# Performance work log

Measured on AMD Instinct MI355X. Metric: run time of the kernel, lower is better.

Reference implementation:

```python
import jax, jax.numpy as jnp
import numpy as np

EPS = 1e-5
WBIT = 4
ABIT = 4

def _ste_round(x):
    return x + jax.lax.stop_gradient(jnp.round(x) - x)

def quantize_k(x, k):
    # uniform quantization to 2^k - 1 levels in [0,1], straight-through round
    n = float(2 ** k - 1)
    return _ste_round(x * n) / n

def weight_quant(w, k=WBIT):
    # DoReFa weight quantization (percentile=1.0 -> plain max)
    t = jnp.tanh(w)
    m = jnp.max(jnp.abs(t))
    wn = t / (2.0 * m) + 0.5            # in [0,1]
    return 2.0 * quantize_k(wn, k) - 1.0  # in [-1,1]

def act_quant(x, k=ABIT):
    return quantize_k(jnp.clip(x, 0.0, 1.0), k)

def bn(x, g, b, m, v):
    # inference batchnorm, per-channel (NCHW)
    scale = g / jnp.sqrt(v + EPS)
    return x * scale[None, :, None, None] + (b - m * scale)[None, :, None, None]

def conv(x, w, stride=1, pad=0, groups=1):
    return jax.lax.conv_general_dilated(
        x, w, window_strides=(stride, stride), padding=[(pad, pad), (pad, pad)],
        feature_group_count=groups, dimension_numbers=('NCHW', 'OIHW', 'NCHW'))

def setup_inputs() -> dict:
    key = jax.random.key(0)
    ks = jax.random.split(key, 17)
    N, Cin, H, W = 32, 64, 56, 56
    hidden = Cin * 6  # 384
    Cout = 64
    d = {
        'x':  jax.random.normal(ks[0], (N, Cin, H, W), jnp.float32),
        'w1': jax.random.normal(ks[1], (hidden, Cin, 1, 1), jnp.float32) * 0.1,
        'w2': jax.random.normal(ks[2], (hidden, 1, 3, 3), jnp.float32) * 0.1,
        'w3': jax.random.normal(ks[3], (Cout, hidden, 1, 1), jnp.float32) * 0.1,
        'g1': jax.random.uniform(ks[4], (hidden,), jnp.float32, 0.5, 1.5),
        'b1': jax.random.normal(ks[5], (hidden,), jnp.float32) * 0.1,
        'm1': jax.random.normal(ks[6], (hidden,), jnp.float32) * 0.1,
        'v1': jax.random.uniform(ks[7], (hidden,), jnp.float32, 0.5, 1.5),
        'g2': jax.random.uniform(ks[8], (hidden,), jnp.float32, 0.5, 1.5),
        'b2': jax.random.normal(ks[9], (hidden,), jnp.float32) * 0.1,
        'm2': jax.random.normal(ks[10], (hidden,), jnp.float32) * 0.1,
        'v2': jax.random.uniform(ks[11], (hidden,), jnp.float32, 0.5, 1.5),
        'g3': jax.random.uniform(ks[12], (Cout,), jnp.float32, 0.5, 1.5),
        'b3': jax.random.normal(ks[13], (Cout,), jnp.float32) * 0.1,
        'm3': jax.random.normal(ks[14], (Cout,), jnp.float32) * 0.1,
        'v3': jax.random.uniform(ks[15], (Cout,), jnp.float32, 0.5, 1.5),
    }
    return d

def reference(x, w1, w2, w3, g1, b1, m1, v1, g2, b2, m2, v2, g3, b3, m3, v3):
    hidden = w1.shape[0]
    shortcut = x
    h = act_quant(jax.nn.relu(bn(conv(x, weight_quant(w1)), g1, b1, m1, v1)))
    h = act_quant(jax.nn.relu(bn(conv(h, weight_quant(w2), stride=1, pad=1, groups=hidden), g2, b2, m2, v2)))
    h = act_quant(bn(conv(h, weight_quant(w3)), g3, b3, m3, v3))
    return h + shortcut  # stride==1 and in_planes==out_planes -> residual
```

## Files before the change

### kernel.cpp

```cpp
#include <hip/hip_runtime.h>
#include <hip/hip_bf16.h>

#define EPS 1e-5f
#define INV15 (1.0f/15.0f)

#define NB 32
#define CIN 64
#define HID 384
#define HH 56
#define HW 3136
#define NPIX 100352
#define BLKPB 1605632
#define NPIXU4 401408

#define OFF_BLOB1 0
#define OFF_W2PK 52224
#define OFF_A2   59136
#define OFF_B2   60672
#define OFF_BLOB3 62208
#define OFF_MAX  87296
#define OFF_H1 1048576
#define OFF_H2 20316160

typedef int v4i __attribute__((ext_vector_type(4)));
typedef float f32x4 __attribute__((ext_vector_type(4)));
typedef short bf16x8 __attribute__((ext_vector_type(8)));

__device__ __forceinline__ short splitbf(float f, float& rem) {
  __hip_bfloat16 h = __float2bfloat16(f);
  rem = f - __bfloat162float(h);
  return __builtin_bit_cast(short, h);
}

__device__ __forceinline__ int pk_mad(unsigned int w, int a, int c) {
  int d;
  asm("v_pk_mad_i16 %0, %1, %2, %3" : "=v"(d) : "v"(w), "v"(a), "v"(c));
  return d;
}

__device__ __forceinline__ int ch_of(int g, int j, int h) {
  return 32 * (g >> 2) + 4 * (g & 3) + 16 * (j & 1) + ((j >> 1) & 1) + 2 * h;
}

__global__ __launch_bounds__(256) void prep_max(
    const float* __restrict__ w1, const float* __restrict__ w2,
    const float* __restrict__ w3, unsigned int* __restrict__ maxout) {
  int b = blockIdx.x >> 4;
  int sub = blockIdx.x & 15;
  const float* src = (b == 0) ? w1 : (b == 1) ? w2 : w3;
  int n = (b == 1) ? HID * 9 : HID * CIN;
  float m = 0.f;
  for (int i = sub * 256 + threadIdx.x; i < n; i += 4096)
    m = fmaxf(m, fabsf(src[i]));
  #pragma unroll
  for (int off = 32; off > 0; off >>= 1)
    m = fmaxf(m, __shfl_down(m, off, 64));
  __shared__ float red[4];
  if ((threadIdx.x & 63) == 0) red[threadIdx.x >> 6] = m;
  __syncthreads();
  if (threadIdx.x == 0) {
    m = fmaxf(fmaxf(red[0], red[1]), fmaxf(red[2], red[3]));
    atomicMax(maxout + b, __float_as_uint(m));
  }
}

__global__ __launch_bounds__(256) void prep_quant(
    const float* __restrict__ w1, const float* __restrict__ w2,
    const float* __restrict__ w3,
    const float* __restrict__ g1, const float* __restrict__ b1,
    const float* __restrict__ m1, const float* __restrict__ v1,
    const float* __restrict__ g2, const float* __restrict__ b2,
    const float* __restrict__ m2, const float* __restrict__ v2,
    const float* __restrict__ g3, const float* __restrict__ b3,
    const float* __restrict__ m3, const float* __restrict__ v3,
    char* __restrict__ ws) {
  const float* maxv = (const float*)(ws + OFF_MAX);
  int idx = blockIdx.x * 256 + threadIdx.x;
  if (idx < 24576) {
    float mm = tanhf(maxv[0]);
    int e = idx & 7, lane = (idx >> 3) & 63, ks = (idx >> 9) & 1, mt = idx >> 10;
    int o = mt * 16 + (lane & 15);
    int k = ks * 32 + (lane >> 4) * 8 + e;
    float t = tanhf(w1[o * 64 + k]);
    int wi = 2 * (int)rintf((t / (2.f * mm) + 0.5f) * 15.f) - 15;
    float rr;
    ((short*)(ws + OFF_BLOB1))[idx] = splitbf((float)wi, rr);
  } else if (idx < 26304) {
    float mm = tanhf(maxv[1]);
    int jj = idx - 24576;
    int tap = jj / 192, rem = jj - tap * 192;
    int g = rem >> 2, j = rem & 3;
    int clo = ch_of(g, j, 0), chi = ch_of(g, j, 1);
    int wlo = 2 * (int)rintf((tanhf(w2[clo * 9 + tap]) / (2.f * mm) + 0.5f) * 15.f) - 15;
    int whi = 2 * (int)rintf((tanhf(w2[chi * 9 + tap]) / (2.f * mm) + 0.5f) * 15.f) - 15;
    ((unsigned int*)(ws + OFF_W2PK))[jj] =
        ((unsigned int)(unsigned short)(short)wlo) |
        (((unsigned int)(unsigned short)(short)whi) << 16);
  } else if (idx < 26688) {
    int ii = idx - 26304;
    int g = ii >> 3, j = (ii >> 1) & 3, h = ii & 1;
    int c = ch_of(g, j, h);
    float s = g2[c] / sqrtf(v2[c] + EPS);
    ((float*)(ws + OFF_A2))[ii] = s * (1.f / 15.f);
  } else if (idx < 27072) {
    int ii = idx - 26688;
    int g = ii >> 3, j = (ii >> 1) & 3, h = ii & 1;
    int c = ch_of(g, j, h);
    float s = g2[c] / sqrtf(v2[c] + EPS);
    ((float*)(ws + OFF_B2))[ii] = 15.f * (b2[c] - m2[c] * s) + 0.5f;
  } else if (idx < 27456) {
    int o = idx - 27072;
    ((float*)(ws + OFF_BLOB1 + 49152))[o] = g1[o] / sqrtf(v1[o] + EPS);
  } else if (idx < 27840) {
    int o = idx - 27456;
    float s = g1[o] / sqrtf(v1[o] + EPS);
    ((float*)(ws + OFF_BLOB1 + 50688))[o] = 15.f * (b1[o] - m1[o] * s);
  } else if (idx < 52416) {
    float mm = tanhf(maxv[2]);
    int jj = idx - 27840;
    int j = jj & 7, lane = (jj >> 3) & 63, nt = (jj >> 9) & 3, ks = jj >> 11;
    int n = nt * 16 + (lane & 15);
    int quad = lane >> 4;
    int k = ks * 32 + ((j & 1) ? (16 + quad * 4 + (j >> 1)) : (quad * 4 + (j >> 1)));
    float t = tanhf(w3[n * 384 + k]);
    int wi = 2 * (int)rintf((t / (2.f * mm) + 0.5f) * 15.f) - 15;
    (ws + OFF_BLOB3)[jj] = (char)wi;
  } else if (idx < 52480) {
    int n = idx - 52416;
    float s = g3[n] / sqrtf(v3[n] + EPS);
    *(float*)(ws + OFF_BLOB3 + 24576 + n * 4) = s * (1.f / 225.f);
  } else if (idx < 52544) {
    int n = idx - 52480;
    float s = g3[n] / sqrtf(v3[n] + EPS);
    *(float*)(ws + OFF_BLOB3 + 24832 + n * 4) = b3[n] - m3[n] * s;
  }
}

__global__ __launch_bounds__(256) void k1(
    const float* __restrict__ x, const char* __restrict__ blob1,
    char* __restrict__ h1b) {
  __shared__ uint4 sBuf[3264];
  int tid = threadIdx.x;
  {
    const uint4* src = (const uint4*)blob1;
    for (int i = tid; i < 3264; i += 256) sBuf[i] = src[i];
  }
  __syncthreads();
  const bf16x8* wf = (const bf16x8*)sBuf;
  const float* sSB = (const float*)(sBuf + 3072);

  int wv = tid >> 6, lane = tid & 63;
  int quad = lane >> 4, m = lane & 15;
  size_t pixabs = (size_t)blockIdx.x * 64 + wv * 16 + m;
  int img = blockIdx.x / 49;
  int prem = (blockIdx.x - img * 49) * 64 + wv * 16 + m;
  const float* xb = x + (size_t)img * (CIN * HW) + prem;

  bf16x8 xh[2], xl[2], xq[2];
  #pragma unroll
  for (int ks = 0; ks < 2; ks++) {
    #pragma unroll
    for (int e = 0; e < 8; e++) {
      float f = xb[(size_t)(ks * 32 + quad * 8 + e) * HW];
      float r1, r2, r3;
      xh[ks][e] = splitbf(f, r1);
      xl[ks][e] = splitbf(r1, r2);
      xq[ks][e] = splitbf(r2, r3);
    }
  }

  #pragma unroll
  for (int half = 0; half < 2; half++) {
    f32x4 acc[12];
    #pragma unroll
    for (int i = 0; i < 12; i++) { f32x4 z = {0.f, 0.f, 0.f, 0.f}; acc[i] = z; }
    #pragma unroll
    for (int i = 0; i < 12; i++) {
      int mt = half * 12 + i;
      bf16x8 w0 = wf[(mt * 2 + 0) * 64 + lane];
      bf16x8 w1 = wf[(mt * 2 + 1) * 64 + lane];
      acc[i] = __builtin_amdgcn_mfma_f32_16x16x32_bf16(w0, xh[0], acc[i], 0, 0, 0);
      acc[i] = __builtin_amdgcn_mfma_f32_16x16x32_bf16(w1, xh[1], acc[i], 0, 0, 0);
      acc[i] = __builtin_amdgcn_mfma_f32_16x16x32_bf16(w0, xl[0], acc[i], 0, 0, 0);
      acc[i] = __builtin_amdgcn_mfma_f32_16x16x32_bf16(w1, xl[1], acc[i], 0, 0, 0);
      acc[i] = __builtin_amdgcn_mfma_f32_16x16x32_bf16(w0, xq[0], acc[i], 0, 0, 0);
      acc[i] = __builtin_amdgcn_mfma_f32_16x16x32_bf16(w1, xq[1], acc[i], 0, 0, 0);
    }
    #pragma unroll
    for (int l = 0; l < 6; l++) {
      int b = half * 6 + l;
      f32x4 ae = acc[2 * l], ao = acc[2 * l + 1];
      unsigned int pk = 0;
      #pragma unroll
      for (int r = 0; r < 4; r++) {
        int oe = 32 * b + quad * 4 + r;
        int oo = oe + 16;
        float fe = fminf(fmaxf(ae[r] * sSB[oe] + sSB[384 + oe], 0.f), 15.f);
        float fo = fminf(fmaxf(ao[r] * sSB[oo] + sSB[384 + oo], 0.f), 15.f);
        pk |= ((unsigned int)(int)rintf(fe)) << (8 * r);
        pk |= ((unsigned int)(int)rintf(fo)) << (8 * r + 4);
      }
      *(unsigned int*)(h1b + (size_t)b * BLKPB + pixabs * 16 + quad * 4) = pk;
    }
  }
}

__global__ __launch_bounds__(256) void k2(
    const unsigned int* __restrict__ h1q, const char* __restrict__ wsrc,
    unsigned int* __restrict__ h2q) {
  __shared__ unsigned int sbuf[2496];
  int tid = threadIdx.x;
  for (int i = tid; i < 2496; i += 256) sbuf[i] = ((const unsigned int*)wsrc)[i];
  __syncthreads();
  const uint4* W4 = (const uint4*)sbuf;
  const float* Af = (const float*)(sbuf + 1728);
  const float* Bf = Af + 384;

  int g = blockIdx.y * 16 + (tid & 15);
  int qid = tid >> 4;
  int img = blockIdx.x / 49;
  int trem = blockIdx.x - img * 49;
  int px0 = trem * 64 + qid * 4;
  int h = px0 / 56;
  int w0 = px0 - h * 56;
  size_t base_u = (size_t)(g >> 2) * NPIXU4 + (g & 3);
  size_t imgrow = (size_t)img * HW;

  int acc[4][4];
  #pragma unroll
  for (int p = 0; p < 4; p++)
    #pragma unroll
    for (int j = 0; j < 4; j++) acc[p][j] = 0;

  #pragma unroll
  for (int dh = 0; dh < 3; dh++) {
    int hr = h + dh - 1;
    bool vrow = (unsigned)hr < 56u;
    const unsigned int* rp = h1q + base_u + (imgrow + (size_t)hr * 56) * 4;
    int P[6][4];
    #pragma unroll
    for (int c = 0; c < 6; c++) {
      int wc = w0 + c - 1;
      unsigned int u = 0;
      if (vrow && (unsigned)wc < 56u) u = rp[(size_t)wc * 4];
      P[c][0] = (int)(u & 0x000F000Fu);
      P[c][1] = (int)((u >> 4) & 0x000F000Fu);
      P[c][2] = (int)((u >> 8) & 0x000F000Fu);
      P[c][3] = (int)((u >> 12) & 0x000F000Fu);
    }
    #pragma unroll
    for (int cw = 0; cw < 3; cw++) {
      uint4 wvv = W4[(dh * 3 + cw) * 48 + g];
      #pragma unroll
      for (int p = 0; p < 4; p++) {
        acc[p][0] = pk_mad(wvv.x, P[p + cw][0], acc[p][0]);
        acc[p][1] = pk_mad(wvv.y, P[p + cw][1], acc[p][1]);
        acc[p][2] = pk_mad(wvv.z, P[p + cw][2], acc[p][2]);
        acc[p][3] = pk_mad(wvv.w, P[p + cw][3], acc[p][3]);
      }
    }
  }

  float Ar[8], Br[8];
  #pragma unroll
  for (int i = 0; i < 8; i++) { Ar[i] = Af[g * 8 + i]; Br[i] = Bf[g * 8 + i]; }

  #pragma unroll
  for (int p = 0; p < 4; p++) {
    unsigned int pk = 0;
    #pragma unroll
    for (int j = 0; j < 4; j++) {
      int a = acc[p][j];
      int lo = (a << 16) >> 16;
      int hi = a >> 16;
      float vl = fmaf((float)lo, Ar[2 * j], Br[2 * j]);
      float vh = fmaf((float)hi, Ar[2 * j + 1], Br[2 * j + 1]);
      unsigned int ql = (unsigned int)fmaxf(fminf(vl, 15.49f), 0.f);
      unsigned int qh = (unsigned int)fmaxf(fminf(vh, 15.49f), 0.f);
      pk |= ql << (4 * j);
      pk |= qh << (4 * j + 16);
    }
    h2q[base_u + (imgrow + (size_t)px0 + p) * 4] = pk;
  }
}

__global__ __launch_bounds__(256) void InvertedBottleneck_conv_Q_13709535609694_kernel(
    const unsigned int* __restrict__ h2q, const char* __restrict__ blob,
    const float* __restrict__ x, float* __restrict__ out) {
  __shared__ long lds8[3136];
  int tid = threadIdx.x;
  {
    const long* src = (const long*)blob;
    #pragma unroll
    for (int i = 0; i < 13; i++) {
      int j = tid + i * 256;
      if (j < 3136) lds8[j] = src[j];
    }
  }
  __syncthreads();

  int wv = tid >> 6;
  int lane = tid & 63;
  int m = lane & 15;
  int quad = lane >> 4;
  int pixW = blockIdx.x * 64 + wv * 16;

  const unsigned int* aptr = h2q + (size_t)(pixW + m) * 4 + quad;
  unsigned int ua[12];
  #pragma unroll
  for (int ks = 0; ks < 12; ks++) ua[ks] = aptr[(size_t)ks * NPIXU4];

  v4i acc[4];
  #pragma unroll
  for (int nt = 0; nt < 4; nt++) { v4i z = {0,0,0,0}; acc[nt] = z; }

  #pragma unroll
  for (int ks = 0; ks < 12; ks++) {
    unsigned int u = ua[ks];
    unsigned int t = u & 0x0F0F0F0Fu;
    unsigned int s = (u >> 4) & 0x0F0F0F0Fu;
    unsigned int d0 = (t & 0xFFu) | ((s & 0xFFu) << 8) | ((t & 0xFF00u) << 8) | ((s & 0xFF00u) << 16);
    unsigned int d1 = ((t >> 16) & 0xFFu) | (((s >> 16) & 0xFFu) << 8) | ((t >> 24) << 16) | ((s >> 24) << 24);
    long aF = (long)(((unsigned long)d1 << 32) | (unsigned long)d0);
    #pragma unroll
    for (int nt = 0; nt < 4; nt++) {
      long bF = lds8[(ks * 4 + nt) * 64 + lane];
      acc[nt] = __builtin_amdgcn_mfma_i32_16x16x32_i8(aF, bF, acc[nt], 0, 0, 0);
    }
  }

  const float* scl = (const float*)(lds8 + 3072);
  int img = blockIdx.x / 49;
  int prem = (blockIdx.x - img * 49) * 64 + wv * 16 + quad * 4;

  #pragma unroll
  for (int nt = 0; nt < 4; nt++) {
    int n = nt * 16 + m;
    float sc = scl[n];
    float bi = scl[64 + n];
    size_t off = ((size_t)img * CIN + n) * HW + prem;
    const float4 xv = *(const float4*)(x + off);
    float4 ov;
    float v, a;
    v = (float)acc[nt][0] * sc + bi; a = fminf(fmaxf(v, 0.f), 1.f); ov.x = rintf(a * 15.f) * INV15 + xv.x;
    v = (float)acc[nt][1] * sc + bi; a = fminf(fmaxf(v, 0.f), 1.f); ov.y = rintf(a * 15.f) * INV15 + xv.y;
    v = (float)acc[nt][2] * sc + bi; a = fminf(fmaxf(v, 0.f), 1.f); ov.z = rintf(a * 15.f) * INV15 + xv.z;
    v = (float)acc[nt][3] * sc + bi; a = fminf(fmaxf(v, 0.f), 1.f); ov.w = rintf(a * 15.f) * INV15 + xv.w;
    *(float4*)(out + off) = ov;
  }
}

extern "C" void kernel_launch(void* const* d_in, const int* in_sizes, int n_in,
                              void* d_out, int out_size, void* d_ws, size_t ws_size,
                              hipStream_t stream) {
  const float* x  = (const float*)d_in[0];
  const float* w1 = (const float*)d_in[1];
  const float* w2 = (const float*)d_in[2];
  const float* w3 = (const float*)d_in[3];
  const float* g1 = (const float*)d_in[4];
  const float* b1 = (const float*)d_in[5];
  const float* m1 = (const float*)d_in[6];
  const float* v1 = (const float*)d_in[7];
  const float* g2 = (const float*)d_in[8];
  const float* b2 = (const float*)d_in[9];
  const float* m2 = (const float*)d_in[10];
  const float* v2 = (const float*)d_in[11];
  const float* g3 = (const float*)d_in[12];
  const float* b3 = (const float*)d_in[13];
  const float* m3 = (const float*)d_in[14];
  const float* v3 = (const float*)d_in[15];

  char* ws = (char*)d_ws;
  unsigned int* maxu = (unsigned int*)(ws + OFF_MAX);
  char* h1b = ws + OFF_H1;
  char* h2b = ws + OFF_H2;
  float* outp = (float*)d_out;

  hipMemsetAsync(maxu, 0, 12, stream);
  prep_max<<<dim3(48), dim3(256), 0, stream>>>(w1, w2, w3, maxu);
  prep_quant<<<dim3(206), dim3(256), 0, stream>>>(
      w1, w2, w3, g1, b1, m1, v1, g2, b2, m2, v2, g3, b3, m3, v3, ws);
  k1<<<dim3(1568), dim3(256), 0, stream>>>(x, ws + OFF_BLOB1, h1b);
  k2<<<dim3(1568, 3), dim3(256), 0, stream>>>(
      (const unsigned int*)h1b, ws + OFF_W2PK, (unsigned int*)h2b);
  InvertedBottleneck_conv_Q_13709535609694_kernel<<<dim3(1568), dim3(256), 0, stream>>>(
      (const unsigned int*)h2b, ws + OFF_BLOB3, x, outp);
}
```

Before: 170.2 us.

## Fuse expand, depthwise and project stages into one kernel with LDS halo tiles

Replaces the three kernels (1x1 expand, 3x3 depthwise, 1x1 project) with one fused kernel. Each block handles two output rows of one image and recomputes a one-row halo above and below for the expand stage. The 4-bit hidden activations stay in shared memory instead of going through global workspace buffers. This removes the global write and read of h1 and h2 and two launches, at the cost of redundant halo compute, only 896 blocks, heavy register use (24 weight fragments, 48 B fragments) and extra barriers.

```diff
diff --git a/kernel.cpp b/kernel.cpp
--- a/kernel.cpp
+++ b/kernel.cpp
@@ -4,14 +4,9 @@
 #define EPS 1e-5f
 #define INV15 (1.0f/15.0f)
 
-#define NB 32
 #define CIN 64
 #define HID 384
-#define HH 56
 #define HW 3136
-#define NPIX 100352
-#define BLKPB 1605632
-#define NPIXU4 401408
 
 #define OFF_BLOB1 0
 #define OFF_W2PK 52224
@@ -19,8 +14,12 @@
 #define OFF_B2   60672
 #define OFF_BLOB3 62208
 #define OFF_MAX  87296
-#define OFF_H1 1048576
-#define OFF_H2 20316160
+
+#define SH_H1 0
+#define SH_K2 11200
+#define SH_S1 13696
+#define SH_SC3 14464
+#define SH_TOT 14592
 
 typedef int v4i __attribute__((ext_vector_type(4)));
 typedef float f32x4 __attribute__((ext_vector_type(4)));
@@ -136,217 +135,220 @@
   }
 }
 
-__global__ __launch_bounds__(256) void k1(
-    const float* __restrict__ x, const char* __restrict__ blob1,
-    char* __restrict__ h1b) {
-  __shared__ uint4 sBuf[3264];
+__global__ __launch_bounds__(256, 2) void InvertedBottleneck_conv_Q_13709535609694_kernel(
+    const float* __restrict__ x, const char* __restrict__ ws,
+    float* __restrict__ out) {
+  __shared__ unsigned int sh[SH_TOT];
   int tid = threadIdx.x;
   {
-    const uint4* src = (const uint4*)blob1;
-    for (int i = tid; i < 3264; i += 256) sBuf[i] = src[i];
-  }
-  __syncthreads();
-  const bf16x8* wf = (const bf16x8*)sBuf;
-  const float* sSB = (const float*)(sBuf + 3072);
+    const unsigned int* s2 = (const unsigned int*)(ws + OFF_W2PK);
+    for (int i = tid; i < 2496; i += 256) sh[SH_K2 + i] = s2[i];
+    const unsigned int* s1 = (const unsigned int*)(ws + OFF_BLOB1 + 49152);
+    for (int i = tid; i < 768; i += 256) sh[SH_S1 + i] = s1[i];
+    const unsigned int* s3 = (const unsigned int*)(ws + OFF_BLOB3 + 24576);
+    if (tid < 128) sh[SH_SC3 + tid] = s3[tid];
+  }
 
   int wv = tid >> 6, lane = tid & 63;
   int quad = lane >> 4, m = lane & 15;
-  size_t pixabs = (size_t)blockIdx.x * 64 + wv * 16 + m;
-  int img = blockIdx.x / 49;
-  int prem = (blockIdx.x - img * 49) * 64 + wv * 16 + m;
-  const float* xb = x + (size_t)img * (CIN * HW) + prem;
-
-  bf16x8 xh[2], xl[2], xq[2];
+  int img = blockIdx.x / 28;
+  int tileid = blockIdx.x - img * 28;
+  int r0 = tileid * 2;
+
+  const float* xb = x + (size_t)img * (CIN * HW);
+  const bf16x8* w1g = (const bf16x8*)(ws + OFF_BLOB1);
+
+  __syncthreads();
+
+  const float* sc15 = (const float*)&sh[SH_S1];
   #pragma unroll
-  for (int ks = 0; ks < 2; ks++) {
-    #pragma unroll
-    for (int e = 0; e < 8; e++) {
-      float f = xb[(size_t)(ks * 32 + quad * 8 + e) * HW];
-      float r1, r2, r3;
-      xh[ks][e] = splitbf(f, r1);
-      xl[ks][e] = splitbf(r1, r2);
-      xq[ks][e] = splitbf(r2, r3);
-    }
-  }
-
-  #pragma unroll
-  for (int half = 0; half < 2; half++) {
-    f32x4 acc[12];
-    #pragma unroll
-    for (int i = 0; i < 12; i++) { f32x4 z = {0.f, 0.f, 0.f, 0.f}; acc[i] = z; }
+  for (int mh = 0; mh < 2; mh++) {
+    bf16x8 wfr[24];
     #pragma unroll
     for (int i = 0; i < 12; i++) {
-      int mt = half * 12 + i;
-      bf16x8 w0 = wf[(mt * 2 + 0) * 64 + lane];
-      bf16x8 w1 = wf[(mt * 2 + 1) * 64 + lane];
-      acc[i] = __builtin_amdgcn_mfma_f32_16x16x32_bf16(w0, xh[0], acc[i], 0, 0, 0);
-      acc[i] = __builtin_amdgcn_mfma_f32_16x16x32_bf16(w1, xh[1], acc[i], 0, 0, 0);
-      acc[i] = __builtin_amdgcn_mfma_f32_16x16x32_bf16(w0, xl[0], acc[i], 0, 0, 0);
-      acc[i] = __builtin_amdgcn_mfma_f32_16x16x32_bf16(w1, xl[1], acc[i], 0, 0, 0);
-      acc[i] = __builtin_amdgcn_mfma_f32_16x16x32_bf16(w0, xq[0], acc[i], 0, 0, 0);
-      acc[i] = __builtin_amdgcn_mfma_f32_16x16x32_bf16(w1, xq[1], acc[i], 0, 0, 0);
+      wfr[2 * i]     = w1g[((mh * 12 + i) * 2 + 0) * 64 + lane];
+      wfr[2 * i + 1] = w1g[((mh * 12 + i) * 2 + 1) * 64 + lane];
     }
+    for (int it = 0; it < 4; it++) {
+      int tile = wv + 4 * it;
+      int px_local = tile * 16 + m;
+      int gpx = r0 * 56 - 56 + px_local;
+      gpx = (gpx < 0) ? 0 : ((gpx > HW - 1) ? HW - 1 : gpx);
+      bf16x8 xh[2], xl[2], xq[2];
+      #pragma unroll
+      for (int ks = 0; ks < 2; ks++) {
+        #pragma unroll
+        for (int e = 0; e < 8; e++) {
+          float f = xb[(size_t)(ks * 32 + quad * 8 + e) * HW + gpx];
+          float r1, r2, r3;
+          xh[ks][e] = splitbf(f, r1);
+          xl[ks][e] = splitbf(r1, r2);
+          xq[ks][e] = splitbf(r2, r3);
+        }
+      }
+      f32x4 acc[12];
+      #pragma unroll
+      for (int i = 0; i < 12; i++) { f32x4 z = {0.f, 0.f, 0.f, 0.f}; acc[i] = z; }
+      #pragma unroll
+      for (int i = 0; i < 12; i++) acc[i] = __builtin_amdgcn_mfma_f32_16x16x32_bf16(wfr[2*i],   xh[0], acc[i], 0, 0, 0);
+      #pragma unroll
+      for (int i = 0; i < 12; i++) acc[i] = __builtin_amdgcn_mfma_f32_16x16x32_bf16(wfr[2*i+1], xh[1], acc[i], 0, 0, 0);
+      #pragma unroll
+      for (int i = 0; i < 12; i++) acc[i] = __builtin_amdgcn_mfma_f32_16x16x32_bf16(wfr[2*i],   xl[0], acc[i], 0, 0, 0);
+      #pragma unroll
+      for (int i = 0; i < 12; i++) acc[i] = __builtin_amdgcn_mfma_f32_16x16x32_bf16(wfr[2*i+1], xl[1], acc[i], 0, 0, 0);
+      #pragma unroll
+      for (int i = 0; i < 12; i++) acc[i] = __builtin_amdgcn_mfma_f32_16x16x32_bf16(wfr[2*i],   xq[0], acc[i], 0, 0, 0);
+      #pragma unroll
+      for (int i = 0; i < 12; i++) acc[i] = __builtin_amdgcn_mfma_f32_16x16x32_bf16(wfr[2*i+1], xq[1], acc[i], 0, 0, 0);
+      if (px_local < 224) {
+        #pragma unroll
+        for (int l = 0; l < 6; l++) {
+          int b = mh * 6 + l;
+          f32x4 ae = acc[2 * l], ao = acc[2 * l + 1];
+          unsigned int pk = 0;
+          #pragma unroll
+          for (int r = 0; r < 4; r++) {
+            int oe = 32 * b + quad * 4 + r;
+            int oo = oe + 16;
+            float fe = fminf(fmaxf(ae[r] * sc15[oe] + sc15[384 + oe], 0.f), 15.f);
+            float fo = fminf(fmaxf(ao[r] * sc15[oo] + sc15[384 + oo], 0.f), 15.f);
+            pk |= ((unsigned int)(int)rintf(fe)) << (8 * r);
+            pk |= ((unsigned int)(int)rintf(fo)) << (8 * r + 4);
+          }
+          sh[SH_H1 + px_local * 50 + b * 4 + quad] = pk;
+        }
+      }
+    }
+  }
+  __syncthreads();
+
+  {
+    const uint4* W4 = (const uint4*)&sh[SH_K2];
+    const float* Af = (const float*)&sh[SH_K2 + 1728];
+    const float* Bf = Af + 384;
     #pragma unroll
-    for (int l = 0; l < 6; l++) {
-      int b = half * 6 + l;
-      f32x4 ae = acc[2 * l], ao = acc[2 * l + 1];
-      unsigned int pk = 0;
-      #pragma unroll
-      for (int r = 0; r < 4; r++) {
-        int oe = 32 * b + quad * 4 + r;
-        int oo = oe + 16;
-        float fe = fminf(fmaxf(ae[r] * sSB[oe] + sSB[384 + oe], 0.f), 15.f);
-        float fo = fminf(fmaxf(ao[r] * sSB[oo] + sSB[384 + oo], 0.f), 15.f);
-        pk |= ((unsigned int)(int)rintf(fe)) << (8 * r);
-        pk |= ((unsigned int)(int)rintf(fo)) << (8 * r + 4);
-      }
-      *(unsigned int*)(h1b + (size_t)b * BLKPB + pixabs * 16 + quad * 4) = pk;
+    for (int orow = 0; orow < 2; orow++) {
+      unsigned int opk[3][4];
+      #pragma unroll
+      for (int it2 = 0; it2 < 3; it2++) {
+        int id = it2 * 256 + tid;
+        int gg = id % 48, q = id / 48;
+        bool act = id < 672;
+        int col = q * 4;
+        int acc2[4][4];
+        #pragma unroll
+        for (int p = 0; p < 4; p++)
+          #pragma unroll
+          for (int j = 0; j < 4; j++) acc2[p][j] = 0;
+        #pragma unroll
+        for (int dh = 0; dh < 3; dh++) {
+          int grow = r0 - 1 + orow + dh;
+          bool vrow = (unsigned)grow < 56u;
+          int P[6][4];
+          #pragma unroll
+          for (int c = 0; c < 6; c++) {
+            int wc = col + c - 1;
+            unsigned int u = 0;
+            if (act && vrow && (unsigned)wc < 56u)
+              u = sh[SH_H1 + ((orow + dh) * 56 + wc) * 50 + gg];
+            P[c][0] = (int)(u & 0x000F000Fu);
+            P[c][1] = (int)((u >> 4) & 0x000F000Fu);
+            P[c][2] = (int)((u >> 8) & 0x000F000Fu);
+            P[c][3] = (int)((u >> 12) & 0x000F000Fu);
+          }
+          #pragma unroll
+          for (int cw = 0; cw < 3; cw++) {
+            uint4 wvv = W4[(dh * 3 + cw) * 48 + gg];
+            #pragma unroll
+            for (int p = 0; p < 4; p++) {
+              acc2[p][0] = pk_mad(wvv.x, P[p + cw][0], acc2[p][0]);
+              acc2[p][1] = pk_mad(wvv.y, P[p + cw][1], acc2[p][1]);
+              acc2[p][2] = pk_mad(wvv.z, P[p + cw][2], acc2[p][2]);
+              acc2[p][3] = pk_mad(wvv.w, P[p + cw][3], acc2[p][3]);
+            }
+          }
+        }
+        float Ar[8], Br[8];
+        #pragma unroll
+        for (int i = 0; i < 8; i++) { Ar[i] = Af[gg * 8 + i]; Br[i] = Bf[gg * 8 + i]; }
+        #pragma unroll
+        for (int p = 0; p < 4; p++) {
+          unsigned int pk = 0;
+          #pragma unroll
+          for (int j = 0; j < 4; j++) {
+            int a = acc2[p][j];
+            int lo = (a << 16) >> 16;
+            int hi = a >> 16;
+            float vl = fmaf((float)lo, Ar[2 * j], Br[2 * j]);
+            float vh = fmaf((float)hi, Ar[2 * j + 1], Br[2 * j + 1]);
+            unsigned int ql = (unsigned int)fmaxf(fminf(vl, 15.49f), 0.f);
+            unsigned int qh = (unsigned int)fmaxf(fminf(vh, 15.49f), 0.f);
+            pk |= ql << (4 * j);
+            pk |= qh << (4 * j + 16);
+          }
+          opk[it2][p] = pk;
+        }
+      }
+      __syncthreads();
+      #pragma unroll
+      for (int it2 = 0; it2 < 3; it2++) {
+        int id = it2 * 256 + tid;
+        int gg = id % 48, q = id / 48;
+        if (id < 672) {
+          #pragma unroll
+          for (int p = 0; p < 4; p++)
+            sh[SH_H1 + (orow * 56 + q * 4 + p) * 50 + gg] = opk[it2][p];
+        }
+      }
+      __syncthreads();
     }
   }
-}
-
-__global__ __launch_bounds__(256) void k2(
-    const unsigned int* __restrict__ h1q, const char* __restrict__ wsrc,
-    unsigned int* __restrict__ h2q) {
-  __shared__ unsigned int sbuf[2496];
-  int tid = threadIdx.x;
-  for (int i = tid; i < 2496; i += 256) sbuf[i] = ((const unsigned int*)wsrc)[i];
-  __syncthreads();
-  const uint4* W4 = (const uint4*)sbuf;
-  const float* Af = (const float*)(sbuf + 1728);
-  const float* Bf = Af + 384;
-
-  int g = blockIdx.y * 16 + (tid & 15);
-  int qid = tid >> 4;
-  int img = blockIdx.x / 49;
-  int trem = blockIdx.x - img * 49;
-  int px0 = trem * 64 + qid * 4;
-  int h = px0 / 56;
-  int w0 = px0 - h * 56;
-  size_t base_u = (size_t)(g >> 2) * NPIXU4 + (g & 3);
-  size_t imgrow = (size_t)img * HW;
-
-  int acc[4][4];
-  #pragma unroll
-  for (int p = 0; p < 4; p++)
+
+  {
+    const unsigned long long* w3g = (const unsigned long long*)(ws + OFF_BLOB3);
+    long bfr[48];
     #pragma unroll
-    for (int j = 0; j < 4; j++) acc[p][j] = 0;
-
-  #pragma unroll
-  for (int dh = 0; dh < 3; dh++) {
-    int hr = h + dh - 1;
-    bool vrow = (unsigned)hr < 56u;
-    const unsigned int* rp = h1q + base_u + (imgrow + (size_t)hr * 56) * 4;
-    int P[6][4];
-    #pragma unroll
-    for (int c = 0; c < 6; c++) {
-      int wc = w0 + c - 1;
-      unsigned int u = 0;
-      if (vrow && (unsigned)wc < 56u) u = rp[(size_t)wc * 4];
-      P[c][0] = (int)(u & 0x000F000Fu);
-      P[c][1] = (int)((u >> 4) & 0x000F000Fu);
-      P[c][2] = (int)((u >> 8) & 0x000F000Fu);
-      P[c][3] = (int)((u >> 12) & 0x000F000Fu);
+    for (int ci = 0; ci < 48; ci++) bfr[ci] = (long)w3g[ci * 64 + lane];
+    const float* scl = (const float*)&sh[SH_SC3];
+
+    for (int t = wv; t < 7; t += 4) {
+      int px = t * 16 + m;
+      unsigned int ua[12];
+      #pragma unroll
+      for (int ks = 0; ks < 12; ks++) ua[ks] = sh[SH_H1 + px * 50 + ks * 4 + quad];
+      v4i acc3[4];
+      #pragma unroll
+      for (int nt = 0; nt < 4; nt++) { v4i z = {0, 0, 0, 0}; acc3[nt] = z; }
+      #pragma unroll
+      for (int ks = 0; ks < 12; ks++) {
+        unsigned int u = ua[ks];
+        unsigned int tt = u & 0x0F0F0F0Fu;
+        unsigned int ss = (u >> 4) & 0x0F0F0F0Fu;
+        unsigned int d0 = (tt & 0xFFu) | ((ss & 0xFFu) << 8) | ((tt & 0xFF00u) << 8) | ((ss & 0xFF00u) << 16);
+        unsigned int d1 = ((tt >> 16) & 0xFFu) | (((ss >> 16) & 0xFFu) << 8) | ((tt >> 24) << 16) | ((ss >> 24) << 24);
+        long aF = (long)(((unsigned long)d1 << 32) | (unsigned long)d0);
+        #pragma unroll
+        for (int nt = 0; nt < 4; nt++)
+          acc3[nt] = __builtin_amdgcn_mfma_i32_16x16x32_i8(aF, bfr[ks * 4 + nt], acc3[nt], 0, 0, 0);
+      }
+      int prem = r0 * 56 + t * 16 + quad * 4;
+      #pragma unroll
+      for (int nt = 0; nt < 4; nt++) {
+        int n = nt * 16 + m;
+        float sc = scl[n];
+        float bi = scl[64 + n];
+        size_t off = ((size_t)img * CIN + n) * HW + prem;
+        const float4 xv = *(const float4*)(x + off);
+        float4 ov;
+        float v, a;
+        v = (float)acc3[nt][0] * sc + bi; a = fminf(fmaxf(v, 0.f), 1.f); ov.x = rintf(a * 15.f) * INV15 + xv.x;
+        v = (float)acc3[nt][1] * sc + bi; a = fminf(fmaxf(v, 0.f), 1.f); ov.y = rintf(a * 15.f) * INV15 + xv.y;
+        v = (float)acc3[nt][2] * sc + bi; a = fminf(fmaxf(v, 0.f), 1.f); ov.z = rintf(a * 15.f) * INV15 + xv.z;
+        v = (float)acc3[nt][3] * sc + bi; a = fminf(fmaxf(v, 0.f), 1.f); ov.w = rintf(a * 15.f) * INV15 + xv.w;
+        *(float4*)(out + off) = ov;
+      }
     }
-    #pragma unroll
-    for (int cw = 0; cw < 3; cw++) {
-      uint4 wvv = W4[(dh * 3 + cw) * 48 + g];
-      #pragma unroll
-      for (int p = 0; p < 4; p++) {
-        acc[p][0] = pk_mad(wvv.x, P[p + cw][0], acc[p][0]);
-        acc[p][1] = pk_mad(wvv.y, P[p + cw][1], acc[p][1]);
-        acc[p][2] = pk_mad(wvv.z, P[p + cw][2], acc[p][2]);
-        acc[p][3] = pk_mad(wvv.w, P[p + cw][3], acc[p][3]);
-      }
-    }
-  }
-
-  float Ar[8], Br[8];
-  #pragma unroll
-  for (int i = 0; i < 8; i++) { Ar[i] = Af[g * 8 + i]; Br[i] = Bf[g * 8 + i]; }
-
-  #pragma unroll
-  for (int p = 0; p < 4; p++) {
-    unsigned int pk = 0;
-    #pragma unroll
-    for (int j = 0; j < 4; j++) {
-      int a = acc[p][j];
-      int lo = (a << 16) >> 16;
-      int hi = a >> 16;
-      float vl = fmaf((float)lo, Ar[2 * j], Br[2 * j]);
-      float vh = fmaf((float)hi, Ar[2 * j + 1], Br[2 * j + 1]);
-      unsigned int ql = (unsigned int)fmaxf(fminf(vl, 15.49f), 0.f);
-      unsigned int qh = (unsigned int)fmaxf(fminf(vh, 15.49f), 0.f);
-      pk |= ql << (4 * j);
-      pk |= qh << (4 * j + 16);
-    }
-    h2q[base_u + (imgrow + (size_t)px0 + p) * 4] = pk;
-  }
-}
-
-__global__ __launch_bounds__(256) void InvertedBottleneck_conv_Q_13709535609694_kernel(
-    const unsigned int* __restrict__ h2q, const char* __restrict__ blob,
-    const float* __restrict__ x, float* __restrict__ out) {
-  __shared__ long lds8[3136];
-  int tid = threadIdx.x;
-  {
-    const long* src = (const long*)blob;
-    #pragma unroll
-    for (int i = 0; i < 13; i++) {
-      int j = tid + i * 256;
-      if (j < 3136) lds8[j] = src[j];
-    }
-  }
-  __syncthreads();
-
-  int wv = tid >> 6;
-  int lane = tid & 63;
-  int m = lane & 15;
-  int quad = lane >> 4;
-  int pixW = blockIdx.x * 64 + wv * 16;
-
-  const unsigned int* aptr = h2q + (size_t)(pixW + m) * 4 + quad;
-  unsigned int ua[12];
-  #pragma unroll
-  for (int ks = 0; ks < 12; ks++) ua[ks] = aptr[(size_t)ks * NPIXU4];
-
-  v4i acc[4];
-  #pragma unroll
-  for (int nt = 0; nt < 4; nt++) { v4i z = {0,0,0,0}; acc[nt] = z; }
-
-  #pragma unroll
-  for (int ks = 0; ks < 12; ks++) {
-    unsigned int u = ua[ks];
-    unsigned int t = u & 0x0F0F0F0Fu;
-    unsigned int s = (u >> 4) & 0x0F0F0F0Fu;
-    unsigned int d0 = (t & 0xFFu) | ((s & 0xFFu) << 8) | ((t & 0xFF00u) << 8) | ((s & 0xFF00u) << 16);
-    unsigned int d1 = ((t >> 16) & 0xFFu) | (((s >> 16) & 0xFFu) << 8) | ((t >> 24) << 16) | ((s >> 24) << 24);
-    long aF = (long)(((unsigned long)d1 << 32) | (unsigned long)d0);
-    #pragma unroll
-    for (int nt = 0; nt < 4; nt++) {
-      long bF = lds8[(ks * 4 + nt) * 64 + lane];
-      acc[nt] = __builtin_amdgcn_mfma_i32_16x16x32_i8(aF, bF, acc[nt], 0, 0, 0);
-    }
-  }
-
-  const float* scl = (const float*)(lds8 + 3072);
-  int img = blockIdx.x / 49;
-  int prem = (blockIdx.x - img * 49) * 64 + wv * 16 + quad * 4;
-
-  #pragma unroll
-  for (int nt = 0; nt < 4; nt++) {
-    int n = nt * 16 + m;
-    float sc = scl[n];
-    float bi = scl[64 + n];
-    size_t off = ((size_t)img * CIN + n) * HW + prem;
-    const float4 xv = *(const float4*)(x + off);
-    float4 ov;
-    float v, a;
-    v = (float)acc[nt][0] * sc + bi; a = fminf(fmaxf(v, 0.f), 1.f); ov.x = rintf(a * 15.f) * INV15 + xv.x;
-    v = (float)acc[nt][1] * sc + bi; a = fminf(fmaxf(v, 0.f), 1.f); ov.y = rintf(a * 15.f) * INV15 + xv.y;
-    v = (float)acc[nt][2] * sc + bi; a = fminf(fmaxf(v, 0.f), 1.f); ov.z = rintf(a * 15.f) * INV15 + xv.z;
-    v = (float)acc[nt][3] * sc + bi; a = fminf(fmaxf(v, 0.f), 1.f); ov.w = rintf(a * 15.f) * INV15 + xv.w;
-    *(float4*)(out + off) = ov;
   }
 }
 
@@ -372,17 +374,12 @@
 
   char* ws = (char*)d_ws;
   unsigned int* maxu = (unsigned int*)(ws + OFF_MAX);
-  char* h1b = ws + OFF_H1;
-  char* h2b = ws + OFF_H2;
   float* outp = (float*)d_out;
 
   hipMemsetAsync(maxu, 0, 12, stream);
   prep_max<<<dim3(48), dim3(256), 0, stream>>>(w1, w2, w3, maxu);
   prep_quant<<<dim3(206), dim3(256), 0, stream>>>(
       w1, w2, w3, g1, b1, m1, v1, g2, b2, m2, v2, g3, b3, m3, v3, ws);
-  k1<<<dim3(1568), dim3(256), 0, stream>>>(x, ws + OFF_BLOB1, h1b);
-  k2<<<dim3(1568, 3), dim3(256), 0, stream>>>(
-      (const unsigned int*)h1b, ws + OFF_W2PK, (unsigned int*)h2b);
-  InvertedBottleneck_conv_Q_13709535609694_kernel<<<dim3(1568), dim3(256), 0, stream>>>(
-      (const unsigned int*)h2b, ws + OFF_BLOB3, x, outp);
-}
+  InvertedBottleneck_conv_Q_13709535609694_kernel<<<dim3(896), dim3(256), 0, stream>>>(
+      x, ws, outp);
+}
```

Result: slower. 185.0 us (+8.7%).

## Fuse depthwise conv into final pointwise conv via shared-memory h2 tile

Applied to the files above, without the earlier changes.

Merges the depthwise 3x3 kernel into the final 1x1 conv kernel. Each block now computes the 64-pixel, 384-channel h2 tile, stores it in LDS and feeds the int8 MFMA directly, so the h2 intermediate never makes a global-memory round trip. k1 is also changed to process two 16-pixel groups per wave with half the grid, reusing the staged weights. The cost is more LDS per block (about 48KB), which lowers occupancy, plus serialization between the depthwise and MFMA phases within a block.

```diff
diff --git a/kernel.cpp b/kernel.cpp
--- a/kernel.cpp
+++ b/kernel.cpp
@@ -4,10 +4,8 @@
 #define EPS 1e-5f
 #define INV15 (1.0f/15.0f)
 
-#define NB 32
 #define CIN 64
 #define HID 384
-#define HH 56
 #define HW 3136
 #define NPIX 100352
 #define BLKPB 1605632
@@ -20,7 +18,12 @@
 #define OFF_BLOB3 62208
 #define OFF_MAX  87296
 #define OFF_H1 1048576
-#define OFF_H2 20316160
+
+#define SH_W2 0
+#define SH_W3 2496
+#define SH_SC3 8640
+#define SH_H2 8768
+#define SH_TOT 11968
 
 typedef int v4i __attribute__((ext_vector_type(4)));
 typedef float f32x4 __attribute__((ext_vector_type(4)));
@@ -151,202 +154,195 @@
 
   int wv = tid >> 6, lane = tid & 63;
   int quad = lane >> 4, m = lane & 15;
-  size_t pixabs = (size_t)blockIdx.x * 64 + wv * 16 + m;
-  int img = blockIdx.x / 49;
-  int prem = (blockIdx.x - img * 49) * 64 + wv * 16 + m;
-  const float* xb = x + (size_t)img * (CIN * HW) + prem;
-
-  bf16x8 xh[2], xl[2], xq[2];
-  #pragma unroll
-  for (int ks = 0; ks < 2; ks++) {
-    #pragma unroll
-    for (int e = 0; e < 8; e++) {
-      float f = xb[(size_t)(ks * 32 + quad * 8 + e) * HW];
-      float r1, r2, r3;
-      xh[ks][e] = splitbf(f, r1);
-      xl[ks][e] = splitbf(r1, r2);
-      xq[ks][e] = splitbf(r2, r3);
-    }
-  }
-
-  #pragma unroll
-  for (int half = 0; half < 2; half++) {
-    f32x4 acc[12];
-    #pragma unroll
-    for (int i = 0; i < 12; i++) { f32x4 z = {0.f, 0.f, 0.f, 0.f}; acc[i] = z; }
-    #pragma unroll
-    for (int i = 0; i < 12; i++) {
-      int mt = half * 12 + i;
-      bf16x8 w0 = wf[(mt * 2 + 0) * 64 + lane];
-      bf16x8 w1 = wf[(mt * 2 + 1) * 64 + lane];
-      acc[i] = __builtin_amdgcn_mfma_f32_16x16x32_bf16(w0, xh[0], acc[i], 0, 0, 0);
-      acc[i] = __builtin_amdgcn_mfma_f32_16x16x32_bf16(w1, xh[1], acc[i], 0, 0, 0);
-      acc[i] = __builtin_amdgcn_mfma_f32_16x16x32_bf16(w0, xl[0], acc[i], 0, 0, 0);
-      acc[i] = __builtin_amdgcn_mfma_f32_16x16x32_bf16(w1, xl[1], acc[i], 0, 0, 0);
-      acc[i] = __builtin_amdgcn_mfma_f32_16x16x32_bf16(w0, xq[0], acc[i], 0, 0, 0);
-      acc[i] = __builtin_amdgcn_mfma_f32_16x16x32_bf16(w1, xq[1], acc[i], 0, 0, 0);
-    }
-    #pragma unroll
-    for (int l = 0; l < 6; l++) {
-      int b = half * 6 + l;
-      f32x4 ae = acc[2 * l], ao = acc[2 * l + 1];
-      unsigned int pk = 0;
-      #pragma unroll
-      for (int r = 0; r < 4; r++) {
-        int oe = 32 * b + quad * 4 + r;
-        int oo = oe + 16;
-        float fe = fminf(fmaxf(ae[r] * sSB[oe] + sSB[384 + oe], 0.f), 15.f);
-        float fo = fminf(fmaxf(ao[r] * sSB[oo] + sSB[384 + oo], 0.f), 15.f);
-        pk |= ((unsigned int)(int)rintf(fe)) << (8 * r);
-        pk |= ((unsigned int)(int)rintf(fo)) << (8 * r + 4);
-      }
-      *(unsigned int*)(h1b + (size_t)b * BLKPB + pixabs * 16 + quad * 4) = pk;
-    }
-  }
-}
-
-__global__ __launch_bounds__(256) void k2(
-    const unsigned int* __restrict__ h1q, const char* __restrict__ wsrc,
-    unsigned int* __restrict__ h2q) {
-  __shared__ unsigned int sbuf[2496];
+
+  for (int t = 0; t < 2; t++) {
+    int grp = blockIdx.x * 8 + t * 4 + wv;
+    size_t pixabs = (size_t)grp * 16 + m;
+    int img = grp / 196;
+    int prem = (grp - img * 196) * 16 + m;
+    const float* xb = x + (size_t)img * (CIN * HW) + prem;
+
+    bf16x8 xh[2], xl[2], xq[2];
+    #pragma unroll
+    for (int ks = 0; ks < 2; ks++) {
+      #pragma unroll
+      for (int e = 0; e < 8; e++) {
+        float f = xb[(size_t)(ks * 32 + quad * 8 + e) * HW];
+        float r1, r2, r3;
+        xh[ks][e] = splitbf(f, r1);
+        xl[ks][e] = splitbf(r1, r2);
+        xq[ks][e] = splitbf(r2, r3);
+      }
+    }
+
+    #pragma unroll
+    for (int half = 0; half < 2; half++) {
+      f32x4 acc[12];
+      #pragma unroll
+      for (int i = 0; i < 12; i++) { f32x4 z = {0.f, 0.f, 0.f, 0.f}; acc[i] = z; }
+      #pragma unroll
+      for (int i = 0; i < 12; i++) {
+        int mt = half * 12 + i;
+        bf16x8 w0 = wf[(mt * 2 + 0) * 64 + lane];
+        bf16x8 w1 = wf[(mt * 2 + 1) * 64 + lane];
+        acc[i] = __builtin_amdgcn_mfma_f32_16x16x32_bf16(w0, xh[0], acc[i], 0, 0, 0);
+        acc[i] = __builtin_amdgcn_mfma_f32_16x16x32_bf16(w1, xh[1], acc[i], 0, 0, 0);
+        acc[i] = __builtin_amdgcn_mfma_f32_16x16x32_bf16(w0, xl[0], acc[i], 0, 0, 0);
+        acc[i] = __builtin_amdgcn_mfma_f32_16x16x32_bf16(w1, xl[1], acc[i], 0, 0, 0);
+        acc[i] = __builtin_amdgcn_mfma_f32_16x16x32_bf16(w0, xq[0], acc[i], 0, 0, 0);
+        acc[i] = __builtin_amdgcn_mfma_f32_16x16x32_bf16(w1, xq[1], acc[i], 0, 0, 0);
+      }
+      #pragma unroll
+      for (int l = 0; l < 6; l++) {
+        int b = half * 6 + l;
+        f32x4 ae = acc[2 * l], ao = acc[2 * l + 1];
+        unsigned int pk = 0;
+        #pragma unroll
+        for (int r = 0; r < 4; r++) {
+          int oe = 32 * b + quad * 4 + r;
+          int oo = oe + 16;
+          float fe = fminf(fmaxf(ae[r] * sSB[oe] + sSB[384 + oe], 0.f), 15.f);
+          float fo = fminf(fmaxf(ao[r] * sSB[oo] + sSB[384 + oo], 0.f), 15.f);
+          pk |= ((unsigned int)(int)rintf(fe)) << (8 * r);
+          pk |= ((unsigned int)(int)rintf(fo)) << (8 * r + 4);
+        }
+        *(unsigned int*)(h1b + (size_t)b * BLKPB + pixabs * 16 + quad * 4) = pk;
+      }
+    }
+  }
+}
+
+__global__ __launch_bounds__(256) void InvertedBottleneck_conv_Q_13709535609694_kernel(
+    const unsigned int* __restrict__ h1q, const char* __restrict__ ws,
+    const float* __restrict__ x, float* __restrict__ out) {
+  __shared__ unsigned int sh[SH_TOT];
   int tid = threadIdx.x;
-  for (int i = tid; i < 2496; i += 256) sbuf[i] = ((const unsigned int*)wsrc)[i];
+  {
+    const unsigned int* s2 = (const unsigned int*)(ws + OFF_W2PK);
+    for (int i = tid; i < 2496; i += 256) sh[SH_W2 + i] = s2[i];
+    const unsigned int* s3 = (const unsigned int*)(ws + OFF_BLOB3);
+    for (int i = tid; i < 6272; i += 256) sh[SH_W3 + i] = s3[i];
+  }
   __syncthreads();
-  const uint4* W4 = (const uint4*)sbuf;
-  const float* Af = (const float*)(sbuf + 1728);
-  const float* Bf = Af + 384;
-
-  int g = blockIdx.y * 16 + (tid & 15);
-  int qid = tid >> 4;
+
   int img = blockIdx.x / 49;
   int trem = blockIdx.x - img * 49;
-  int px0 = trem * 64 + qid * 4;
-  int h = px0 / 56;
-  int w0 = px0 - h * 56;
-  size_t base_u = (size_t)(g >> 2) * NPIXU4 + (g & 3);
   size_t imgrow = (size_t)img * HW;
 
-  int acc[4][4];
-  #pragma unroll
-  for (int p = 0; p < 4; p++)
-    #pragma unroll
-    for (int j = 0; j < 4; j++) acc[p][j] = 0;
-
-  #pragma unroll
-  for (int dh = 0; dh < 3; dh++) {
-    int hr = h + dh - 1;
-    bool vrow = (unsigned)hr < 56u;
-    const unsigned int* rp = h1q + base_u + (imgrow + (size_t)hr * 56) * 4;
-    int P[6][4];
-    #pragma unroll
-    for (int c = 0; c < 6; c++) {
-      int wc = w0 + c - 1;
-      unsigned int u = 0;
-      if (vrow && (unsigned)wc < 56u) u = rp[(size_t)wc * 4];
-      P[c][0] = (int)(u & 0x000F000Fu);
-      P[c][1] = (int)((u >> 4) & 0x000F000Fu);
-      P[c][2] = (int)((u >> 8) & 0x000F000Fu);
-      P[c][3] = (int)((u >> 12) & 0x000F000Fu);
-    }
-    #pragma unroll
-    for (int cw = 0; cw < 3; cw++) {
-      uint4 wvv = W4[(dh * 3 + cw) * 48 + g];
+  {
+    const uint4* W4 = (const uint4*)&sh[SH_W2];
+    const float* Af = (const float*)&sh[SH_W2 + 1728];
+    const float* Bf = Af + 384;
+    #pragma unroll
+    for (int it2 = 0; it2 < 3; it2++) {
+      int id = it2 * 256 + tid;
+      int gg = id % 48, q4 = id / 48;
+      int prem = trem * 64 + q4 * 4;
+      int h = prem / 56, w0 = prem - h * 56;
+      size_t base_u = (size_t)(gg >> 2) * NPIXU4 + (gg & 3);
+      int acc2[4][4];
+      #pragma unroll
+      for (int p = 0; p < 4; p++)
+        #pragma unroll
+        for (int j = 0; j < 4; j++) acc2[p][j] = 0;
+      #pragma unroll
+      for (int dh = 0; dh < 3; dh++) {
+        int hr = h + dh - 1;
+        bool vrow = (unsigned)hr < 56u;
+        const unsigned int* rp = h1q + base_u + (imgrow + (size_t)hr * 56) * 4;
+        int P[6][4];
+        #pragma unroll
+        for (int c = 0; c < 6; c++) {
+          int wc = w0 + c - 1;
+          unsigned int u = 0;
+          if (vrow && (unsigned)wc < 56u) u = rp[(size_t)wc * 4];
+          P[c][0] = (int)(u & 0x000F000Fu);
+          P[c][1] = (int)((u >> 4) & 0x000F000Fu);
+          P[c][2] = (int)((u >> 8) & 0x000F000Fu);
+          P[c][3] = (int)((u >> 12) & 0x000F000Fu);
+        }
+        #pragma unroll
+        for (int cw = 0; cw < 3; cw++) {
+          uint4 wvv = W4[(dh * 3 + cw) * 48 + gg];
+          #pragma unroll
+          for (int p = 0; p < 4; p++) {
+            acc2[p][0] = pk_mad(wvv.x, P[p + cw][0], acc2[p][0]);
+            acc2[p][1] = pk_mad(wvv.y, P[p + cw][1], acc2[p][1]);
+            acc2[p][2] = pk_mad(wvv.z, P[p + cw][2], acc2[p][2]);
+            acc2[p][3] = pk_mad(wvv.w, P[p + cw][3], acc2[p][3]);
+          }
+        }
+      }
+      float Ar[8], Br[8];
+      #pragma unroll
+      for (int i = 0; i < 8; i++) { Ar[i] = Af[gg * 8 + i]; Br[i] = Bf[gg * 8 + i]; }
       #pragma unroll
       for (int p = 0; p < 4; p++) {
-        acc[p][0] = pk_mad(wvv.x, P[p + cw][0], acc[p][0]);
-        acc[p][1] = pk_mad(wvv.y, P[p + cw][1], acc[p][1]);
-        acc[p][2] = pk_mad(wvv.z, P[p + cw][2], acc[p][2]);
-        acc[p][3] = pk_mad(wvv.w, P[p + cw][3], acc[p][3]);
-      }
-    }
-  }
-
-  float Ar[8], Br[8];
-  #pragma unroll
-  for (int i = 0; i < 8; i++) { Ar[i] = Af[g * 8 + i]; Br[i] = Bf[g * 8 + i]; }
-
-  #pragma unroll
-  for (int p = 0; p < 4; p++) {
-    unsigned int pk = 0;
-    #pragma unroll
-    for (int j = 0; j < 4; j++) {
-      int a = acc[p][j];
-      int lo = (a << 16) >> 16;
-      int hi = a >> 16;
-      float vl = fmaf((float)lo, Ar[2 * j], Br[2 * j]);
-      float vh = fmaf((float)hi, Ar[2 * j + 1], Br[2 * j + 1]);
-      unsigned int ql = (unsigned int)fmaxf(fminf(vl, 15.49f), 0.f);
-      unsigned int qh = (unsigned int)fmaxf(fminf(vh, 15.49f), 0.f);
-      pk |= ql << (4 * j);
-      pk |= qh << (4 * j + 16);
-    }
-    h2q[base_u + (imgrow + (size_t)px0 + p) * 4] = pk;
-  }
-}
-
-__global__ __launch_bounds__(256) void InvertedBottleneck_conv_Q_13709535609694_kernel(
-    const unsigned int* __restrict__ h2q, const char* __restrict__ blob,
-    const float* __restrict__ x, float* __restrict__ out) {
-  __shared__ long lds8[3136];
-  int tid = threadIdx.x;
+        unsigned int pk = 0;
+        #pragma unroll
+        for (int j = 0; j < 4; j++) {
+          int a = acc2[p][j];
+          int lo = (a << 16) >> 16;
+          int hi = a >> 16;
+          float vl = fmaf((float)lo, Ar[2 * j], Br[2 * j]);
+          float vh = fmaf((float)hi, Ar[2 * j + 1], Br[2 * j + 1]);
+          unsigned int ql = (unsigned int)fmaxf(fminf(vl, 15.49f), 0.f);
+          unsigned int qh = (unsigned int)fmaxf(fminf(vh, 15.49f), 0.f);
+          pk |= ql << (4 * j);
+          pk |= qh << (4 * j + 16);
+        }
+        sh[SH_H2 + (q4 * 4 + p) * 50 + gg] = pk;
+      }
+    }
+  }
+  __syncthreads();
+
   {
-    const long* src = (const long*)blob;
-    #pragma unroll
-    for (int i = 0; i < 13; i++) {
-      int j = tid + i * 256;
-      if (j < 3136) lds8[j] = src[j];
-    }
-  }
-  __syncthreads();
-
-  int wv = tid >> 6;
-  int lane = tid & 63;
-  int m = lane & 15;
-  int quad = lane >> 4;
-  int pixW = blockIdx.x * 64 + wv * 16;
-
-  const unsigned int* aptr = h2q + (size_t)(pixW + m) * 4 + quad;
-  unsigned int ua[12];
-  #pragma unroll
-  for (int ks = 0; ks < 12; ks++) ua[ks] = aptr[(size_t)ks * NPIXU4];
-
-  v4i acc[4];
-  #pragma unroll
-  for (int nt = 0; nt < 4; nt++) { v4i z = {0,0,0,0}; acc[nt] = z; }
-
-  #pragma unroll
-  for (int ks = 0; ks < 12; ks++) {
-    unsigned int u = ua[ks];
-    unsigned int t = u & 0x0F0F0F0Fu;
-    unsigned int s = (u >> 4) & 0x0F0F0F0Fu;
-    unsigned int d0 = (t & 0xFFu) | ((s & 0xFFu) << 8) | ((t & 0xFF00u) << 8) | ((s & 0xFF00u) << 16);
-    unsigned int d1 = ((t >> 16) & 0xFFu) | (((s >> 16) & 0xFFu) << 8) | ((t >> 24) << 16) | ((s >> 24) << 24);
-    long aF = (long)(((unsigned long)d1 << 32) | (unsigned long)d0);
+    int wv = tid >> 6, lane = tid & 63;
+    int m = lane & 15, quad = lane >> 4;
+    const long* sh8 = (const long*)&sh[SH_W3];
+    const float* scl = (const float*)&sh[SH_SC3];
+    int px_local = wv * 16 + m;
+
+    unsigned int ua[12];
+    #pragma unroll
+    for (int ks = 0; ks < 12; ks++) ua[ks] = sh[SH_H2 + px_local * 50 + ks * 4 + quad];
+
+    v4i acc3[4];
+    #pragma unroll
+    for (int nt = 0; nt < 4; nt++) { v4i z = {0, 0, 0, 0}; acc3[nt] = z; }
+
+    #pragma unroll
+    for (int ks = 0; ks < 12; ks++) {
+      unsigned int u = ua[ks];
+      unsigned int tt = u & 0x0F0F0F0Fu;
+      unsigned int ss = (u >> 4) & 0x0F0F0F0Fu;
+      unsigned int d0 = (tt & 0xFFu) | ((ss & 0xFFu) << 8) | ((tt & 0xFF00u) << 8) | ((ss & 0xFF00u) << 16);
+      unsigned int d1 = ((tt >> 16) & 0xFFu) | (((ss >> 16) & 0xFFu) << 8) | ((tt >> 24) << 16) | ((ss >> 24) << 24);
+      long aF = (long)(((unsigned long)d1 << 32) | (unsigned long)d0);
+      #pragma unroll
+      for (int nt = 0; nt < 4; nt++) {
+        long bF = sh8[(ks * 4 + nt) * 64 + lane];
+        acc3[nt] = __builtin_amdgcn_mfma_i32_16x16x32_i8(aF, bF, acc3[nt], 0, 0, 0);
+      }
+    }
+
+    int prem = trem * 64 + wv * 16 + quad * 4;
     #pragma unroll
     for (int nt = 0; nt < 4; nt++) {
-      long bF = lds8[(ks * 4 + nt) * 64 + lane];
-      acc[nt] = __builtin_amdgcn_mfma_i32_16x16x32_i8(aF, bF, acc[nt], 0, 0, 0);
-    }
-  }
-
-  const float* scl = (const float*)(lds8 + 3072);
-  int img = blockIdx.x / 49;
-  int prem = (blockIdx.x - img * 49) * 64 + wv * 16 + quad * 4;
-
-  #pragma unroll
-  for (int nt = 0; nt < 4; nt++) {
-    int n = nt * 16 + m;
-    float sc = scl[n];
-    float bi = scl[64 + n];
-    size_t off = ((size_t)img * CIN + n) * HW + prem;
-    const float4 xv = *(const float4*)(x + off);
-    float4 ov;
-    float v, a;
-    v = (float)acc[nt][0] * sc + bi; a = fminf(fmaxf(v, 0.f), 1.f); ov.x = rintf(a * 15.f) * INV15 + xv.x;
-    v = (float)acc[nt][1] * sc + bi; a = fminf(fmaxf(v, 0.f), 1.f); ov.y = rintf(a * 15.f) * INV15 + xv.y;
-    v = (float)acc[nt][2] * sc + bi; a = fminf(fmaxf(v, 0.f), 1.f); ov.z = rintf(a * 15.f) * INV15 + xv.z;
-    v = (float)acc[nt][3] * sc + bi; a = fminf(fmaxf(v, 0.f), 1.f); ov.w = rintf(a * 15.f) * INV15 + xv.w;
-    *(float4*)(out + off) = ov;
+      int n = nt * 16 + m;
+      float sc = scl[n];
+      float bi = scl[64 + n];
+      size_t off = ((size_t)img * CIN + n) * HW + prem;
+      const float4 xv = *(const float4*)(x + off);
+      float4 ov;
+      float v, a;
+      v = (float)acc3[nt][0] * sc + bi; a = fminf(fmaxf(v, 0.f), 1.f); ov.x = rintf(a * 15.f) * INV15 + xv.x;
+      v = (float)acc3[nt][1] * sc + bi; a = fminf(fmaxf(v, 0.f), 1.f); ov.y = rintf(a * 15.f) * INV15 + xv.y;
+      v = (float)acc3[nt][2] * sc + bi; a = fminf(fmaxf(v, 0.f), 1.f); ov.z = rintf(a * 15.f) * INV15 + xv.z;
+      v = (float)acc3[nt][3] * sc + bi; a = fminf(fmaxf(v, 0.f), 1.f); ov.w = rintf(a * 15.f) * INV15 + xv.w;
+      *(float4*)(out + off) = ov;
+    }
   }
 }
 
@@ -373,16 +369,13 @@
   char* ws = (char*)d_ws;
   unsigned int* maxu = (unsigned int*)(ws + OFF_MAX);
   char* h1b = ws + OFF_H1;
-  char* h2b = ws + OFF_H2;
   float* outp = (float*)d_out;
 
   hipMemsetAsync(maxu, 0, 12, stream);
   prep_max<<<dim3(48), dim3(256), 0, stream>>>(w1, w2, w3, maxu);
   prep_quant<<<dim3(206), dim3(256), 0, stream>>>(
       w1, w2, w3, g1, b1, m1, v1, g2, b2, m2, v2, g3, b3, m3, v3, ws);
-  k1<<<dim3(1568), dim3(256), 0, stream>>>(x, ws + OFF_BLOB1, h1b);
-  k2<<<dim3(1568, 3), dim3(256), 0, stream>>>(
-      (const unsigned int*)h1b, ws + OFF_W2PK, (unsigned int*)h2b);
+  k1<<<dim3(784), dim3(256), 0, stream>>>(x, ws + OFF_BLOB1, h1b);
   InvertedBottleneck_conv_Q_13709535609694_kernel<<<dim3(1568), dim3(256), 0, stream>>>(
-      (const unsigned int*)h2b, ws + OFF_BLOB3, x, outp);
-}
+      (const unsigned int*)h1b, ws, x, outp);
+}
```

Result: slower. 201.0 us (+18.1%).
